# Optimization experiments

Hardware: AMD Instinct MI355X
Metric: run time of the kernel (lower is better)

The kernel has to match this reference:

```python
import jax, jax.numpy as jnp
import numpy as np
import math

B, Q_LEN, K_LEN = 8, 512, 512
D_MODEL, H = 512, 8
DK = D_MODEL // H


def setup_inputs() -> dict:
    key = jax.random.key(0)
    ks = jax.random.split(key, 12)
    inp = {
        "query": jax.random.normal(ks[0], (B, Q_LEN, D_MODEL), jnp.float32),
        "key": jax.random.normal(ks[1], (B, K_LEN, D_MODEL), jnp.float32),
        "value": jax.random.normal(ks[2], (B, K_LEN, D_MODEL), jnp.float32),
        "relative_embeddings": jax.random.normal(ks[3], (K_LEN, Q_LEN, D_MODEL), jnp.float32),
        # causal mask: 1 = attend, 0 = masked
        "mask": jnp.tril(jnp.ones((Q_LEN, K_LEN), dtype=bool)),
        "Wq": jax.random.normal(ks[4], (D_MODEL, D_MODEL), jnp.float32) / math.sqrt(D_MODEL),
        "Wk": jax.random.normal(ks[5], (D_MODEL, D_MODEL), jnp.float32) / math.sqrt(D_MODEL),
        "Wv": jax.random.normal(ks[6], (D_MODEL, D_MODEL), jnp.float32) / math.sqrt(D_MODEL),
        "Wo": jax.random.normal(ks[7], (D_MODEL, D_MODEL), jnp.float32) / math.sqrt(D_MODEL),
        "Wr": jax.random.normal(ks[8], (D_MODEL, D_MODEL), jnp.float32) / math.sqrt(D_MODEL),
        "u": jax.random.normal(ks[9], (H, DK), jnp.float32),
        "v": jax.random.normal(ks[10], (H, DK), jnp.float32),
    }
    return inp


def reference(query, key, value, relative_embeddings, mask, Wq, Wk, Wv, Wo, Wr, u, v):
    b, q_len, d_model = query.shape
    k_len = key.shape[1]
    # torch nn.Linear(x) = x @ W.T (bias=False)
    Qh = (query @ Wq.T).reshape(b, q_len, H, DK).transpose(0, 2, 1, 3)   # bhqd
    Kh = (key @ Wk.T).reshape(b, k_len, H, DK).transpose(0, 2, 1, 3)     # bhkd
    Vh = (value @ Wv.T).reshape(b, k_len, H, DK).transpose(0, 2, 1, 3)   # bhkd
    # relative position projection: (k_len, q_len, d_model)
    R = relative_embeddings @ Wr.T
    # view(k,q,H,dk).permute(2,1,0,3) -> (H, q, k, dk)
    Rh = R.reshape(k_len, q_len, H, DK).transpose(2, 1, 0, 3)
    # content score: (Q + u) K^T
    content = jnp.einsum("bhqd,bhkd->bhqk", Qh + u[None, :, None, :], Kh)
    # position score: (Q + v) R^T, R per-head per-query
    position = jnp.einsum("bhqd,hqkd->bhqk", Qh + v[None, :, None, :], Rh)
    scores = (content + position) / math.sqrt(DK)
    scores = jnp.where(mask[None, None, :, :], scores, -1e9)
    weights = jax.nn.softmax(scores, axis=-1)  # dropout is identity in eval
    out = jnp.einsum("bhqk,bhkd->bhqd", weights, Vh)
    out = out.transpose(0, 2, 1, 3).reshape(b, q_len, d_model)
    out = out @ Wo.T
    return (out, weights)
```

## Files before the change

### kernel.cpp

```cpp
#include <hip/hip_runtime.h>

#define BATCH   8
#define SEQ     512
#define DMODEL  512
#define NHEAD   8
#define DKH     64

typedef __attribute__((ext_vector_type(8))) short bf16x8;
typedef __attribute__((ext_vector_type(4))) float f32x4;

__device__ __forceinline__ short f2bf(float f) {
    union { float f; unsigned u; } v; v.f = f;
    unsigned r = v.u + 0x7FFFu + ((v.u >> 16) & 1u);
    return (short)(r >> 16);
}
__device__ __forceinline__ float bf2f(short s) {
    union { unsigned u; float f; } v; v.u = ((unsigned)(unsigned short)s) << 16;
    return v.f;
}

#define LDK 40

__device__ __forceinline__ void stage_f32(const float* __restrict__ base,
                                          int rstride, short* lds, int tid) {
    int r = tid >> 2, c = (tid & 3) << 3;
    const float* p = base + (size_t)r * rstride + c;
    float4 x = *(const float4*)p;
    float4 y = *(const float4*)(p + 4);
    union { short s[8]; bf16x8 v; } o;
    o.s[0] = f2bf(x.x); o.s[1] = f2bf(x.y); o.s[2] = f2bf(x.z); o.s[3] = f2bf(x.w);
    o.s[4] = f2bf(y.x); o.s[5] = f2bf(y.y); o.s[6] = f2bf(y.z); o.s[7] = f2bf(y.w);
    *(bf16x8*)(lds + r * LDK + c) = o.v;
}

__device__ __forceinline__ void stage_bf16(const short* __restrict__ base,
                                           int rstride, short* lds, int tid) {
    int r = tid >> 2, c = (tid & 3) << 3;
    bf16x8 v = *(const bf16x8*)(base + (size_t)r * rstride + c);
    *(bf16x8*)(lds + r * LDK + c) = v;
}

__device__ __forceinline__ void mma_tile(const short* As, const short* Bs,
                                         int lane, int wm, int wn, f32x4 acc[2][2]) {
    int lo = lane & 15, hi = lane >> 4;
    bf16x8 a0 = *(const bf16x8*)(As + (wm * 32 + lo) * LDK + hi * 8);
    bf16x8 a1 = *(const bf16x8*)(As + (wm * 32 + 16 + lo) * LDK + hi * 8);
    bf16x8 b0 = *(const bf16x8*)(Bs + (wn * 32 + lo) * LDK + hi * 8);
    bf16x8 b1 = *(const bf16x8*)(Bs + (wn * 32 + 16 + lo) * LDK + hi * 8);
    acc[0][0] = __builtin_amdgcn_mfma_f32_16x16x32_bf16(a0, b0, acc[0][0], 0, 0, 0);
    acc[0][1] = __builtin_amdgcn_mfma_f32_16x16x32_bf16(a0, b1, acc[0][1], 0, 0, 0);
    acc[1][0] = __builtin_amdgcn_mfma_f32_16x16x32_bf16(a1, b0, acc[1][0], 0, 0, 0);
    acc[1][1] = __builtin_amdgcn_mfma_f32_16x16x32_bf16(a1, b1, acc[1][1], 0, 0, 0);
}

__global__ __launch_bounds__(256) void qkvw_kernel(
        const float* __restrict__ query, const float* __restrict__ key_,
        const float* __restrict__ value,
        const float* __restrict__ Wq, const float* __restrict__ Wk,
        const float* __restrict__ Wv, const float* __restrict__ Wr,
        const float* __restrict__ uvec, const float* __restrict__ vvec,
        short* __restrict__ Qu, short* __restrict__ Qv,
        short* __restrict__ Kh, short* __restrict__ Vt,
        short* __restrict__ Wrt) {
    __shared__ short As[64 * LDK], Bs[64 * LDK];
    int f = blockIdx.x, tid = threadIdx.x;
    if (f >= 1536) {
        int base = (f - 1536) * 1024;
        #pragma unroll
        for (int j = 0; j < 4; j++) {
            int idx = base + j * 256 + tid;
            int n = idx >> 9, m = idx & 511;
            Wrt[idx] = f2bf(Wr[(size_t)m * 512 + n]);
        }
        return;
    }
    int i = f >> 3;
    int nt = i & 7;
    int gm = (f & 7) * 24 + (i >> 3);
    int mode = gm >> 6, mt = gm & 63;
    const float* x = mode == 0 ? query : (mode == 1 ? key_ : value);
    const float* W = mode == 0 ? Wq : (mode == 1 ? Wk : Wv);
    int lane = tid & 63, w = tid >> 6, wm = w >> 1, wn = w & 1;
    const float* Abase = x + (size_t)mt * 64 * DMODEL;
    const float* Bbase = W + (size_t)nt * 64 * DMODEL;
    f32x4 acc[2][2] = {};
    for (int kt = 0; kt < DMODEL; kt += 32) {
        __syncthreads();
        stage_f32(Abase + kt, DMODEL, As, tid);
        stage_f32(Bbase + kt, DMODEL, Bs, tid);
        __syncthreads();
        mma_tile(As, Bs, lane, wm, wn, acc);
    }
    int lo = lane & 15, hi = lane >> 4;
    for (int fm = 0; fm < 2; fm++)
        for (int fn = 0; fn < 2; fn++)
            for (int r = 0; r < 4; r++) {
                int m = mt * 64 + wm * 32 + fm * 16 + hi * 4 + r;
                int n = nt * 64 + wn * 32 + fn * 16 + lo;
                float val = acc[fm][fn][r];
                int b = m >> 9, s = m & 511, h = n >> 6, d = n & 63;
                if (mode == 0) {
                    size_t idx = ((size_t)(b * NHEAD + h) * SEQ + s) * DKH + d;
                    Qu[idx] = f2bf(val + uvec[n]);
                    Qv[idx] = f2bf(val + vvec[n]);
                } else if (mode == 1) {
                    Kh[((size_t)(b * NHEAD + h) * SEQ + s) * DKH + d] = f2bf(val);
                } else {
                    Vt[((size_t)(b * NHEAD + h) * DKH + d) * SEQ + s] = f2bf(val);
                }
            }
}

__global__ __launch_bounds__(256) void t_kernel(const short* __restrict__ Qv,
                                                const short* __restrict__ Wrt,
                                                short* __restrict__ T2) {
    __shared__ short As[64 * LDK], Bs[64 * LDK];
    int f = blockIdx.x;
    int i = f >> 3;
    int nt = i & 7;
    int mh = (f & 7) * 64 + (i >> 3);
    int mt = mh >> 3, h = mh & 7;
    int tid = threadIdx.x, lane = tid & 63, w = tid >> 6, wm = w >> 1, wn = w & 1;
    int m0 = mt * 64, b = m0 >> 9, q0 = m0 & 511;
    const short* Abase = Qv + ((size_t)(b * NHEAD + h) * SEQ + q0) * DKH;
    const short* Bbase = Wrt + (size_t)nt * 64 * DMODEL + h * DKH;
    f32x4 acc[2][2] = {};
    for (int kt = 0; kt < DKH; kt += 32) {
        __syncthreads();
        stage_bf16(Abase + kt, DKH, As, tid);
        stage_bf16(Bbase + kt, DMODEL, Bs, tid);
        __syncthreads();
        mma_tile(As, Bs, lane, wm, wn, acc);
    }
    int lo = lane & 15, hi = lane >> 4;
    int bh = b * NHEAD + h;
    for (int fm = 0; fm < 2; fm++)
        for (int fn = 0; fn < 2; fn++)
            for (int r = 0; r < 4; r++) {
                int q = q0 + wm * 32 + fm * 16 + hi * 4 + r;
                int n = nt * 64 + wn * 32 + fn * 16 + lo;
                T2[((size_t)q * 64 + bh) * DMODEL + n] = f2bf(acc[fm][fn][r]);
            }
}

__global__ __launch_bounds__(256) void content_kernel(const short* __restrict__ Qu,
                                                      const short* __restrict__ Kh,
                                                      float* __restrict__ scores) {
    int f = blockIdx.x;
    int i = f >> 3;
    int bh = (f & 7) * 8 + (i >> 6);
    int rest = i & 63;
    int kt_ = rest & 7, qt = rest >> 3;
    if (kt_ > qt) return;
    __shared__ short As[64 * LDK], Bs[64 * LDK];
    int tid = threadIdx.x, lane = tid & 63, w = tid >> 6, wm = w >> 1, wn = w & 1;
    const short* Abase = Qu + ((size_t)bh * SEQ + qt * 64) * DKH;
    const short* Bbase = Kh + ((size_t)bh * SEQ + kt_ * 64) * DKH;
    f32x4 acc[2][2] = {};
    for (int kt = 0; kt < DKH; kt += 32) {
        __syncthreads();
        stage_bf16(Abase + kt, DKH, As, tid);
        stage_bf16(Bbase + kt, DKH, Bs, tid);
        __syncthreads();
        mma_tile(As, Bs, lane, wm, wn, acc);
    }
    int lo = lane & 15, hi = lane >> 4;
    for (int fm = 0; fm < 2; fm++)
        for (int fn = 0; fn < 2; fn++)
            for (int r = 0; r < 4; r++) {
                int q = qt * 64 + wm * 32 + fm * 16 + hi * 4 + r;
                int k = kt_ * 64 + wn * 32 + fn * 16 + lo;
                scores[((size_t)bh * SEQ + q) * SEQ + k] = acc[fm][fn][r];
            }
}

__global__ __launch_bounds__(512) void position_kernel(const short* __restrict__ T2,
                                                       const float* __restrict__ rel,
                                                       float* __restrict__ scores) {
    int bk = blockIdx.x;
    int j = bk >> 3;
    int q = (bk & 7) * 64 + (j >> 1);
    int half = j & 1;
    if (half * 256 > q) return;
    __shared__ short Tl[64 * 512];
    int tid = threadIdx.x, w = tid >> 6, lane = tid & 63;
    const short* Tq = T2 + (size_t)q * (64 * DMODEL);
    #pragma unroll
    for (int it = 0; it < 8; ++it) {
        int chunk = it * 512 + tid;
        int r = chunk >> 6, c = chunk & 63;
        bf16x8 v = *(const bf16x8*)(Tq + (size_t)chunk * 8);
        *(bf16x8*)(Tl + r * 512 + (c ^ (r & 7)) * 8) = v;
    }
    __syncthreads();
    int kbase = half * 256 + w * 32;
    if (kbase > q) return;
    int lo = lane & 15, hi = lane >> 4;
    const float* relq = rel + ((size_t)kbase * SEQ + q) * DMODEL;
    f32x4 acc[4][2] = {};
    for (int n = 0; n < DMODEL; n += 32) {
        bf16x8 a[4];
        #pragma unroll
        for (int fm = 0; fm < 4; fm++) {
            int rr = fm * 16 + lo;
            int g = ((n >> 3) + hi) ^ (rr & 7);
            a[fm] = *(const bf16x8*)(Tl + rr * 512 + g * 8);
        }
        bf16x8 bfrag[2];
        #pragma unroll
        for (int fk = 0; fk < 2; fk++) {
            const float* p = relq + (size_t)(fk * 16 + lo) * (SEQ * DMODEL) + n + hi * 8;
            float4 x = *(const float4*)p;
            float4 y = *(const float4*)(p + 4);
            union { short s[8]; bf16x8 v; } o;
            o.s[0] = f2bf(x.x); o.s[1] = f2bf(x.y); o.s[2] = f2bf(x.z); o.s[3] = f2bf(x.w);
            o.s[4] = f2bf(y.x); o.s[5] = f2bf(y.y); o.s[6] = f2bf(y.z); o.s[7] = f2bf(y.w);
            bfrag[fk] = o.v;
        }
        #pragma unroll
        for (int fm = 0; fm < 4; fm++) {
            acc[fm][0] = __builtin_amdgcn_mfma_f32_16x16x32_bf16(a[fm], bfrag[0], acc[fm][0], 0, 0, 0);
            acc[fm][1] = __builtin_amdgcn_mfma_f32_16x16x32_bf16(a[fm], bfrag[1], acc[fm][1], 0, 0, 0);
        }
    }
    #pragma unroll
    for (int fm = 0; fm < 4; fm++)
        #pragma unroll
        for (int fk = 0; fk < 2; fk++)
            #pragma unroll
            for (int r = 0; r < 4; r++) {
                int bh = fm * 16 + hi * 4 + r;
                int k = kbase + fk * 16 + lo;
                scores[((size_t)bh * SEQ + q) * SEQ + k] += acc[fm][fk][r];
            }
}

__global__ __launch_bounds__(256) void pv_sm_kernel(float* __restrict__ scores,
                                                    const short* __restrict__ Vt,
                                                    short* __restrict__ attn) {
    __shared__ short As[64 * LDK], Bs[64 * LDK];
    int f = blockIdx.x;
    int i = f >> 3;
    int bh = (f & 7) * 8 + (i >> 3);
    int qt = i & 7;
    int tid = threadIdx.x, lane = tid & 63, w = tid >> 6, wm = w >> 1, wn = w & 1;
    int kmax = (qt + 1) * 64;
    int r = tid >> 2, c4 = tid & 3;
    int q = qt * 64 + r;
    float* row = scores + ((size_t)bh * SEQ + q) * SEQ;
    float M = -1e30f, S = 0.f;
    int kbeg = c4 * 128;
    int kend = (kbeg + 128 < kmax) ? kbeg + 128 : kmax;
    for (int k = kbeg; k < kend; k += 4) {
        float4 vv = *(const float4*)(row + k);
        float x0 = (k + 0 <= q) ? vv.x * 0.125f : -1e30f;
        float x1 = (k + 1 <= q) ? vv.y * 0.125f : -1e30f;
        float x2 = (k + 2 <= q) ? vv.z * 0.125f : -1e30f;
        float x3 = (k + 3 <= q) ? vv.w * 0.125f : -1e30f;
        float mx = fmaxf(fmaxf(x0, x1), fmaxf(x2, x3));
        float Mn = fmaxf(M, mx);
        S = S * __expf(M - Mn) + __expf(x0 - Mn) + __expf(x1 - Mn)
          + __expf(x2 - Mn) + __expf(x3 - Mn);
        M = Mn;
    }
    #pragma unroll
    for (int off = 1; off <= 2; off <<= 1) {
        float Mo = __shfl_xor(M, off), So = __shfl_xor(S, off);
        float Mn = fmaxf(M, Mo);
        S = S * __expf(M - Mn) + So * __expf(Mo - Mn);
        M = Mn;
    }
    float invS = 1.0f / S;
    const short* Bbase = Vt + (size_t)bh * DKH * SEQ;
    f32x4 acc[2][2] = {};
    int cc = c4 * 8;
    for (int kt = 0; kt < SEQ; kt += 32) {
        if (kt < kmax) {
            __syncthreads();
            stage_bf16(Bbase + kt, SEQ, Bs, tid);
            float4 x = *(const float4*)(row + kt + cc);
            float4 y = *(const float4*)(row + kt + cc + 4);
            float p0 = (kt + cc + 0 <= q) ? __expf(x.x * 0.125f - M) * invS : 0.f;
            float p1 = (kt + cc + 1 <= q) ? __expf(x.y * 0.125f - M) * invS : 0.f;
            float p2 = (kt + cc + 2 <= q) ? __expf(x.z * 0.125f - M) * invS : 0.f;
            float p3 = (kt + cc + 3 <= q) ? __expf(x.w * 0.125f - M) * invS : 0.f;
            float p4 = (kt + cc + 4 <= q) ? __expf(y.x * 0.125f - M) * invS : 0.f;
            float p5 = (kt + cc + 5 <= q) ? __expf(y.y * 0.125f - M) * invS : 0.f;
            float p6 = (kt + cc + 6 <= q) ? __expf(y.z * 0.125f - M) * invS : 0.f;
            float p7 = (kt + cc + 7 <= q) ? __expf(y.w * 0.125f - M) * invS : 0.f;
            *(float4*)(row + kt + cc) = make_float4(p0, p1, p2, p3);
            *(float4*)(row + kt + cc + 4) = make_float4(p4, p5, p6, p7);
            union { short s[8]; bf16x8 v; } o;
            o.s[0] = f2bf(p0); o.s[1] = f2bf(p1); o.s[2] = f2bf(p2); o.s[3] = f2bf(p3);
            o.s[4] = f2bf(p4); o.s[5] = f2bf(p5); o.s[6] = f2bf(p6); o.s[7] = f2bf(p7);
            *(bf16x8*)(As + r * LDK + cc) = o.v;
            __syncthreads();
            mma_tile(As, Bs, lane, wm, wn, acc);
        } else {
            float4 z = make_float4(0.f, 0.f, 0.f, 0.f);
            *(float4*)(row + kt + cc) = z;
            *(float4*)(row + kt + cc + 4) = z;
        }
    }
    int lo = lane & 15, hi = lane >> 4;
    int b = bh >> 3, h = bh & 7;
    for (int fm = 0; fm < 2; fm++)
        for (int fn = 0; fn < 2; fn++)
            for (int rr = 0; rr < 4; rr++) {
                int qq = qt * 64 + wm * 32 + fm * 16 + hi * 4 + rr;
                int d = wn * 32 + fn * 16 + lo;
                attn[((size_t)b * SEQ + qq) * DMODEL + h * DKH + d] = f2bf(acc[fm][fn][rr]);
            }
}

__global__ __launch_bounds__(256) void oproj_kernel(const short* __restrict__ attn,
                                                    const float* __restrict__ Wo,
                                                    float* __restrict__ out) {
    __shared__ short As[64 * LDK], Bs[64 * LDK];
    int f = blockIdx.x;
    int i = f >> 3;
    int mt = (f & 7) * 8 + (i >> 3);
    int nt = i & 7;
    int tid = threadIdx.x, lane = tid & 63, w = tid >> 6, wm = w >> 1, wn = w & 1;
    const short* Abase = attn + (size_t)mt * 64 * DMODEL;
    const float* Bbase = Wo + (size_t)nt * 64 * DMODEL;
    f32x4 acc[2][2] = {};
    for (int kt = 0; kt < DMODEL; kt += 32) {
        __syncthreads();
        stage_bf16(Abase + kt, DMODEL, As, tid);
        stage_f32(Bbase + kt, DMODEL, Bs, tid);
        __syncthreads();
        mma_tile(As, Bs, lane, wm, wn, acc);
    }
    int lo = lane & 15, hi = lane >> 4;
    for (int fm = 0; fm < 2; fm++)
        for (int fn = 0; fn < 2; fn++)
            for (int r = 0; r < 4; r++) {
                int m = mt * 64 + wm * 32 + fm * 16 + hi * 4 + r;
                int n = nt * 64 + wn * 32 + fn * 16 + lo;
                out[(size_t)m * DMODEL + n] = acc[fm][fn][r];
            }
}

extern "C" void kernel_launch(void* const* d_in, const int* in_sizes, int n_in,
                              void* d_out, int out_size, void* d_ws, size_t ws_size,
                              hipStream_t stream) {
    (void)in_sizes; (void)n_in; (void)out_size; (void)ws_size;
    const float* query = (const float*)d_in[0];
    const float* key   = (const float*)d_in[1];
    const float* value = (const float*)d_in[2];
    const float* rel   = (const float*)d_in[3];
    const float* Wq = (const float*)d_in[5];
    const float* Wk = (const float*)d_in[6];
    const float* Wv = (const float*)d_in[7];
    const float* Wo = (const float*)d_in[8];
    const float* Wr = (const float*)d_in[9];
    const float* u  = (const float*)d_in[10];
    const float* v  = (const float*)d_in[11];

    float* out     = (float*)d_out;
    float* weights = out + (size_t)BATCH * SEQ * DMODEL;

    char* ws = (char*)d_ws;
    short* Qu   = (short*)(ws);
    short* Qv   = (short*)(ws + ((size_t)4 << 20));
    short* Kh   = (short*)(ws + ((size_t)8 << 20));
    short* Vt   = (short*)(ws + ((size_t)12 << 20));
    short* T2   = (short*)(ws + ((size_t)16 << 20));
    short* attn = (short*)(ws + ((size_t)48 << 20));
    short* Wrt  = (short*)(ws + ((size_t)52 << 20));

    qkvw_kernel<<<1792, 256, 0, stream>>>(query, key, value, Wq, Wk, Wv, Wr,
                                          u, v, Qu, Qv, Kh, Vt, Wrt);
    t_kernel<<<4096, 256, 0, stream>>>(Qv, Wrt, T2);
    content_kernel<<<4096, 256, 0, stream>>>(Qu, Kh, weights);
    position_kernel<<<1024, 512, 0, stream>>>(T2, rel, weights);
    pv_sm_kernel<<<512, 256, 0, stream>>>(weights, Vt, attn);
    oproj_kernel<<<512, 256, 0, stream>>>(attn, Wo, out);
}
```

Measured before the change: 222.8 us.

## Fuse content-score QK^T into softmax+PV kernel, recomputing scores in two passes

Removes the separate content_kernel and computes QK^T on the fly inside the softmax/PV kernel. The kernel does a first pass that sums exp-scores and a second pass that recomputes QK^T, normalises, writes the weights and runs PV. The position kernel now writes scores directly instead of read-modify-write, which saves one full read and write of the score tensor. It also remaps the position kernel's q block order. The softmax drops the max subtraction, which risks overflow for large scores, and Q·K is computed twice.

```diff
diff --git a/kernel.cpp b/kernel.cpp
--- a/kernel.cpp
+++ b/kernel.cpp
@@ -13,10 +13,6 @@
     union { float f; unsigned u; } v; v.f = f;
     unsigned r = v.u + 0x7FFFu + ((v.u >> 16) & 1u);
     return (short)(r >> 16);
-}
-__device__ __forceinline__ float bf2f(short s) {
-    union { unsigned u; float f; } v; v.u = ((unsigned)(unsigned short)s) << 16;
-    return v.f;
 }
 
 #define LDK 40
@@ -143,44 +139,13 @@
             }
 }
 
-__global__ __launch_bounds__(256) void content_kernel(const short* __restrict__ Qu,
-                                                      const short* __restrict__ Kh,
-                                                      float* __restrict__ scores) {
-    int f = blockIdx.x;
-    int i = f >> 3;
-    int bh = (f & 7) * 8 + (i >> 6);
-    int rest = i & 63;
-    int kt_ = rest & 7, qt = rest >> 3;
-    if (kt_ > qt) return;
-    __shared__ short As[64 * LDK], Bs[64 * LDK];
-    int tid = threadIdx.x, lane = tid & 63, w = tid >> 6, wm = w >> 1, wn = w & 1;
-    const short* Abase = Qu + ((size_t)bh * SEQ + qt * 64) * DKH;
-    const short* Bbase = Kh + ((size_t)bh * SEQ + kt_ * 64) * DKH;
-    f32x4 acc[2][2] = {};
-    for (int kt = 0; kt < DKH; kt += 32) {
-        __syncthreads();
-        stage_bf16(Abase + kt, DKH, As, tid);
-        stage_bf16(Bbase + kt, DKH, Bs, tid);
-        __syncthreads();
-        mma_tile(As, Bs, lane, wm, wn, acc);
-    }
-    int lo = lane & 15, hi = lane >> 4;
-    for (int fm = 0; fm < 2; fm++)
-        for (int fn = 0; fn < 2; fn++)
-            for (int r = 0; r < 4; r++) {
-                int q = qt * 64 + wm * 32 + fm * 16 + hi * 4 + r;
-                int k = kt_ * 64 + wn * 32 + fn * 16 + lo;
-                scores[((size_t)bh * SEQ + q) * SEQ + k] = acc[fm][fn][r];
-            }
-}
-
 __global__ __launch_bounds__(512) void position_kernel(const short* __restrict__ T2,
                                                        const float* __restrict__ rel,
                                                        float* __restrict__ scores) {
     int bk = blockIdx.x;
-    int j = bk >> 3;
-    int q = (bk & 7) * 64 + (j >> 1);
-    int half = j & 1;
+    int x = bk & 7, idx = bk >> 3;
+    int q = (idx >> 1) * 8 + x;
+    int half = idx & 1;
     if (half * 256 > q) return;
     __shared__ short Tl[64 * 512];
     int tid = threadIdx.x, w = tid >> 6, lane = tid & 63;
@@ -210,11 +175,11 @@
         #pragma unroll
         for (int fk = 0; fk < 2; fk++) {
             const float* p = relq + (size_t)(fk * 16 + lo) * (SEQ * DMODEL) + n + hi * 8;
-            float4 x = *(const float4*)p;
-            float4 y = *(const float4*)(p + 4);
+            float4 xv = *(const float4*)p;
+            float4 yv = *(const float4*)(p + 4);
             union { short s[8]; bf16x8 v; } o;
-            o.s[0] = f2bf(x.x); o.s[1] = f2bf(x.y); o.s[2] = f2bf(x.z); o.s[3] = f2bf(x.w);
-            o.s[4] = f2bf(y.x); o.s[5] = f2bf(y.y); o.s[6] = f2bf(y.z); o.s[7] = f2bf(y.w);
+            o.s[0] = f2bf(xv.x); o.s[1] = f2bf(xv.y); o.s[2] = f2bf(xv.z); o.s[3] = f2bf(xv.w);
+            o.s[4] = f2bf(yv.x); o.s[5] = f2bf(yv.y); o.s[6] = f2bf(yv.z); o.s[7] = f2bf(yv.w);
             bfrag[fk] = o.v;
         }
         #pragma unroll
@@ -231,85 +196,146 @@
             for (int r = 0; r < 4; r++) {
                 int bh = fm * 16 + hi * 4 + r;
                 int k = kbase + fk * 16 + lo;
-                scores[((size_t)bh * SEQ + q) * SEQ + k] += acc[fm][fk][r];
-            }
-}
-
-__global__ __launch_bounds__(256) void pv_sm_kernel(float* __restrict__ scores,
-                                                    const short* __restrict__ Vt,
-                                                    short* __restrict__ attn) {
-    __shared__ short As[64 * LDK], Bs[64 * LDK];
+                scores[((size_t)bh * SEQ + q) * SEQ + k] = acc[fm][fk][r];
+            }
+}
+
+__global__ __launch_bounds__(256) void pv_cs_kernel(
+        const short* __restrict__ Qu, const short* __restrict__ Kh,
+        const short* __restrict__ Vt, float* __restrict__ weights,
+        short* __restrict__ attn) {
+    __shared__ short Ks[2 * 64 * LDK];
+    __shared__ short Vs[2 * 64 * LDK];
+    __shared__ short Ps[2 * 64 * LDK];
+    __shared__ float S_lds[2][64];
+    __shared__ float invS_lds[64];
     int f = blockIdx.x;
     int i = f >> 3;
     int bh = (f & 7) * 8 + (i >> 3);
     int qt = i & 7;
+    int q0 = qt * 64, kmax = q0 + 64;
     int tid = threadIdx.x, lane = tid & 63, w = tid >> 6, wm = w >> 1, wn = w & 1;
-    int kmax = (qt + 1) * 64;
-    int r = tid >> 2, c4 = tid & 3;
-    int q = qt * 64 + r;
-    float* row = scores + ((size_t)bh * SEQ + q) * SEQ;
-    float M = -1e30f, S = 0.f;
-    int kbeg = c4 * 128;
-    int kend = (kbeg + 128 < kmax) ? kbeg + 128 : kmax;
-    for (int k = kbeg; k < kend; k += 4) {
-        float4 vv = *(const float4*)(row + k);
-        float x0 = (k + 0 <= q) ? vv.x * 0.125f : -1e30f;
-        float x1 = (k + 1 <= q) ? vv.y * 0.125f : -1e30f;
-        float x2 = (k + 2 <= q) ? vv.z * 0.125f : -1e30f;
-        float x3 = (k + 3 <= q) ? vv.w * 0.125f : -1e30f;
-        float mx = fmaxf(fmaxf(x0, x1), fmaxf(x2, x3));
-        float Mn = fmaxf(M, mx);
-        S = S * __expf(M - Mn) + __expf(x0 - Mn) + __expf(x1 - Mn)
-          + __expf(x2 - Mn) + __expf(x3 - Mn);
-        M = Mn;
-    }
+    int lo = lane & 15, hi = lane >> 4;
+    bf16x8 aq[2][2];
     #pragma unroll
-    for (int off = 1; off <= 2; off <<= 1) {
-        float Mo = __shfl_xor(M, off), So = __shfl_xor(S, off);
-        float Mn = fmaxf(M, Mo);
-        S = S * __expf(M - Mn) + So * __expf(Mo - Mn);
-        M = Mn;
-    }
-    float invS = 1.0f / S;
-    const short* Bbase = Vt + (size_t)bh * DKH * SEQ;
-    f32x4 acc[2][2] = {};
-    int cc = c4 * 8;
-    for (int kt = 0; kt < SEQ; kt += 32) {
-        if (kt < kmax) {
-            __syncthreads();
-            stage_bf16(Bbase + kt, SEQ, Bs, tid);
-            float4 x = *(const float4*)(row + kt + cc);
-            float4 y = *(const float4*)(row + kt + cc + 4);
-            float p0 = (kt + cc + 0 <= q) ? __expf(x.x * 0.125f - M) * invS : 0.f;
-            float p1 = (kt + cc + 1 <= q) ? __expf(x.y * 0.125f - M) * invS : 0.f;
-            float p2 = (kt + cc + 2 <= q) ? __expf(x.z * 0.125f - M) * invS : 0.f;
-            float p3 = (kt + cc + 3 <= q) ? __expf(x.w * 0.125f - M) * invS : 0.f;
-            float p4 = (kt + cc + 4 <= q) ? __expf(y.x * 0.125f - M) * invS : 0.f;
-            float p5 = (kt + cc + 5 <= q) ? __expf(y.y * 0.125f - M) * invS : 0.f;
-            float p6 = (kt + cc + 6 <= q) ? __expf(y.z * 0.125f - M) * invS : 0.f;
-            float p7 = (kt + cc + 7 <= q) ? __expf(y.w * 0.125f - M) * invS : 0.f;
-            *(float4*)(row + kt + cc) = make_float4(p0, p1, p2, p3);
-            *(float4*)(row + kt + cc + 4) = make_float4(p4, p5, p6, p7);
-            union { short s[8]; bf16x8 v; } o;
-            o.s[0] = f2bf(p0); o.s[1] = f2bf(p1); o.s[2] = f2bf(p2); o.s[3] = f2bf(p3);
-            o.s[4] = f2bf(p4); o.s[5] = f2bf(p5); o.s[6] = f2bf(p6); o.s[7] = f2bf(p7);
-            *(bf16x8*)(As + r * LDK + cc) = o.v;
-            __syncthreads();
-            mma_tile(As, Bs, lane, wm, wn, acc);
-        } else {
+    for (int fm = 0; fm < 2; fm++)
+        #pragma unroll
+        for (int ch = 0; ch < 2; ch++)
+            aq[fm][ch] = *(const bf16x8*)(Qu + ((size_t)bh * SEQ + q0 + wm * 32 + fm * 16 + lo) * DKH + ch * 32 + hi * 8);
+    const short* Khb = Kh + (size_t)bh * SEQ * DKH;
+    const short* Vtb = Vt + (size_t)bh * DKH * SEQ;
+    float Sa[2][4] = {};
+    for (int kt = 0; kt < kmax; kt += 64) {
+        __syncthreads();
+        stage_bf16(Khb + (size_t)kt * DKH,      DKH, Ks,            tid);
+        stage_bf16(Khb + (size_t)kt * DKH + 32, DKH, Ks + 64 * LDK, tid);
+        __syncthreads();
+        f32x4 acc[2][2] = {};
+        #pragma unroll
+        for (int ch = 0; ch < 2; ch++) {
+            bf16x8 b0 = *(const bf16x8*)(Ks + ch * 64 * LDK + (wn * 32 + lo) * LDK + hi * 8);
+            bf16x8 b1 = *(const bf16x8*)(Ks + ch * 64 * LDK + (wn * 32 + 16 + lo) * LDK + hi * 8);
+            #pragma unroll
+            for (int fm = 0; fm < 2; fm++) {
+                acc[fm][0] = __builtin_amdgcn_mfma_f32_16x16x32_bf16(aq[fm][ch], b0, acc[fm][0], 0, 0, 0);
+                acc[fm][1] = __builtin_amdgcn_mfma_f32_16x16x32_bf16(aq[fm][ch], b1, acc[fm][1], 0, 0, 0);
+            }
+        }
+        #pragma unroll
+        for (int fm = 0; fm < 2; fm++)
+            #pragma unroll
+            for (int fn = 0; fn < 2; fn++) {
+                int k = kt + wn * 32 + fn * 16 + lo;
+                #pragma unroll
+                for (int r = 0; r < 4; r++) {
+                    int qq = q0 + wm * 32 + fm * 16 + hi * 4 + r;
+                    float ps = weights[((size_t)bh * SEQ + qq) * SEQ + k];
+                    float xx = (acc[fm][fn][r] + ps) * 0.125f;
+                    float p = (k <= qq) ? __expf(xx) : 0.f;
+                    Sa[fm][r] += p;
+                }
+            }
+    }
+    #pragma unroll
+    for (int fm = 0; fm < 2; fm++)
+        #pragma unroll
+        for (int r = 0; r < 4; r++) {
+            float s = Sa[fm][r];
+            s += __shfl_xor(s, 1); s += __shfl_xor(s, 2);
+            s += __shfl_xor(s, 4); s += __shfl_xor(s, 8);
+            if (lo == 0) S_lds[wn][wm * 32 + fm * 16 + hi * 4 + r] = s;
+        }
+    __syncthreads();
+    if (tid < 64) invS_lds[tid] = 1.0f / (S_lds[0][tid] + S_lds[1][tid]);
+    f32x4 pacc[2][2] = {};
+    for (int kt = 0; kt < kmax; kt += 64) {
+        __syncthreads();
+        stage_bf16(Khb + (size_t)kt * DKH,      DKH, Ks,            tid);
+        stage_bf16(Khb + (size_t)kt * DKH + 32, DKH, Ks + 64 * LDK, tid);
+        stage_bf16(Vtb + kt,      SEQ, Vs,            tid);
+        stage_bf16(Vtb + kt + 32, SEQ, Vs + 64 * LDK, tid);
+        __syncthreads();
+        f32x4 acc[2][2] = {};
+        #pragma unroll
+        for (int ch = 0; ch < 2; ch++) {
+            bf16x8 b0 = *(const bf16x8*)(Ks + ch * 64 * LDK + (wn * 32 + lo) * LDK + hi * 8);
+            bf16x8 b1 = *(const bf16x8*)(Ks + ch * 64 * LDK + (wn * 32 + 16 + lo) * LDK + hi * 8);
+            #pragma unroll
+            for (int fm = 0; fm < 2; fm++) {
+                acc[fm][0] = __builtin_amdgcn_mfma_f32_16x16x32_bf16(aq[fm][ch], b0, acc[fm][0], 0, 0, 0);
+                acc[fm][1] = __builtin_amdgcn_mfma_f32_16x16x32_bf16(aq[fm][ch], b1, acc[fm][1], 0, 0, 0);
+            }
+        }
+        #pragma unroll
+        for (int fm = 0; fm < 2; fm++)
+            #pragma unroll
+            for (int fn = 0; fn < 2; fn++) {
+                int kl = wn * 32 + fn * 16 + lo;
+                int k = kt + kl;
+                #pragma unroll
+                for (int r = 0; r < 4; r++) {
+                    int ql = wm * 32 + fm * 16 + hi * 4 + r;
+                    int qq = q0 + ql;
+                    size_t off = ((size_t)bh * SEQ + qq) * SEQ + k;
+                    float ps = weights[off];
+                    float xx = (acc[fm][fn][r] + ps) * 0.125f;
+                    float p = (k <= qq) ? __expf(xx) * invS_lds[ql] : 0.f;
+                    weights[off] = p;
+                    Ps[wn * 64 * LDK + ql * LDK + fn * 16 + lo] = f2bf(p);
+                }
+            }
+        __syncthreads();
+        #pragma unroll
+        for (int kc = 0; kc < 2; kc++) {
+            bf16x8 bv0 = *(const bf16x8*)(Vs + kc * 64 * LDK + (wn * 32 + lo) * LDK + hi * 8);
+            bf16x8 bv1 = *(const bf16x8*)(Vs + kc * 64 * LDK + (wn * 32 + 16 + lo) * LDK + hi * 8);
+            #pragma unroll
+            for (int fm = 0; fm < 2; fm++) {
+                bf16x8 ap = *(const bf16x8*)(Ps + kc * 64 * LDK + (wm * 32 + fm * 16 + lo) * LDK + hi * 8);
+                pacc[fm][0] = __builtin_amdgcn_mfma_f32_16x16x32_bf16(ap, bv0, pacc[fm][0], 0, 0, 0);
+                pacc[fm][1] = __builtin_amdgcn_mfma_f32_16x16x32_bf16(ap, bv1, pacc[fm][1], 0, 0, 0);
+            }
+        }
+    }
+    {
+        int r = tid >> 2, c0 = (tid & 3) * 16;
+        for (int kz = kmax; kz < SEQ; kz += 64) {
+            float* wr = weights + ((size_t)bh * SEQ + q0 + r) * SEQ + kz + c0;
             float4 z = make_float4(0.f, 0.f, 0.f, 0.f);
-            *(float4*)(row + kt + cc) = z;
-            *(float4*)(row + kt + cc + 4) = z;
-        }
-    }
-    int lo = lane & 15, hi = lane >> 4;
+            *(float4*)(wr) = z; *(float4*)(wr + 4) = z;
+            *(float4*)(wr + 8) = z; *(float4*)(wr + 12) = z;
+        }
+    }
     int b = bh >> 3, h = bh & 7;
-    for (int fm = 0; fm < 2; fm++)
+    #pragma unroll
+    for (int fm = 0; fm < 2; fm++)
+        #pragma unroll
         for (int fn = 0; fn < 2; fn++)
-            for (int rr = 0; rr < 4; rr++) {
-                int qq = qt * 64 + wm * 32 + fm * 16 + hi * 4 + rr;
+            #pragma unroll
+            for (int r = 0; r < 4; r++) {
+                int qq = q0 + wm * 32 + fm * 16 + hi * 4 + r;
                 int d = wn * 32 + fn * 16 + lo;
-                attn[((size_t)b * SEQ + qq) * DMODEL + h * DKH + d] = f2bf(acc[fm][fn][rr]);
+                attn[((size_t)b * SEQ + qq) * DMODEL + h * DKH + d] = f2bf(pacc[fm][fn][r]);
             }
 }
 
@@ -373,8 +399,7 @@
     qkvw_kernel<<<1792, 256, 0, stream>>>(query, key, value, Wq, Wk, Wv, Wr,
                                           u, v, Qu, Qv, Kh, Vt, Wrt);
     t_kernel<<<4096, 256, 0, stream>>>(Qv, Wrt, T2);
-    content_kernel<<<4096, 256, 0, stream>>>(Qu, Kh, weights);
     position_kernel<<<1024, 512, 0, stream>>>(T2, rel, weights);
-    pv_sm_kernel<<<512, 256, 0, stream>>>(weights, Vt, attn);
+    pv_cs_kernel<<<512, 256, 0, stream>>>(Qu, Kh, Vt, weights, attn);
     oproj_kernel<<<512, 256, 0, stream>>>(attn, Wo, out);
 }
```

After: 252.1 us. 1.13x slower.
